# Performance work log

Hardware: AMD Instinct MI355X
Metric: run time of the kernel (lower is better)

## Reference

```python
import jax, jax.numpy as jnp
import numpy as np

B, T, C = 4, 2048, 1024
H, D = 16, 64  # num_heads, head_dim
P = 64         # prefix length


def setup_inputs() -> dict:
    key = jax.random.key(0)
    ks = jax.random.split(key, 12)
    s = 1.0 / np.sqrt(C)
    return {
        "x": jax.random.normal(ks[0], (B, T, C), dtype=jnp.float32),
        "attn_mask": jax.random.randint(ks[1], (B, 1, 1, T), 0, 2, dtype=jnp.int32),
        "prefix_k": jax.random.normal(ks[2], (B, H, P, D), dtype=jnp.float32),
        "prefix_v": jax.random.normal(ks[3], (B, H, P, D), dtype=jnp.float32),
        "Wq": jax.random.normal(ks[4], (C, C), dtype=jnp.float32) * s,
        "bq": jnp.zeros((C,), dtype=jnp.float32),
        "Wk": jax.random.normal(ks[5], (C, C), dtype=jnp.float32) * s,
        "bk": jnp.zeros((C,), dtype=jnp.float32),
        "Wv": jax.random.normal(ks[6], (C, C), dtype=jnp.float32) * s,
        "bv": jnp.zeros((C,), dtype=jnp.float32),
        "Wo": jax.random.normal(ks[7], (C, C), dtype=jnp.float32) * s,
        "bo": jnp.zeros((C,), dtype=jnp.float32),
    }


def _heads(y):
    # [B,T,C] -> [B,H,T,D]
    return y.reshape(B, T, H, D).transpose(0, 2, 1, 3)


def reference(x, attn_mask, prefix_k, prefix_v, Wq, bq, Wk, bk, Wv, bv, Wo, bo):
    q = _heads(x @ Wq.T + bq)
    k = _heads(x @ Wk.T + bk)
    v = _heads(x @ Wv.T + bv)
    # concat prefix K/V along key dim -> [B,H,P+T,D]
    k = jnp.concatenate([prefix_k, k], axis=2)
    v = jnp.concatenate([prefix_v, v], axis=2)
    # prefix positions are always visible
    prefix_mask = jnp.ones((B, 1, 1, P), dtype=attn_mask.dtype)
    mask = jnp.concatenate([prefix_mask, attn_mask], axis=-1)  # [B,1,1,P+T]
    scores = jnp.einsum('bhtd,bhsd->bhts', q, k) / jnp.sqrt(jnp.asarray(D, x.dtype))
    scores = jnp.where(mask == 0, -jnp.inf, scores)
    w = jax.nn.softmax(scores, axis=-1)
    o = jnp.einsum('bhts,bhsd->bhtd', w, v)
    o = o.transpose(0, 2, 1, 3).reshape(B, T, C)
    return o @ Wo.T + bo
```

## Files before the change

kernel.cpp:

```cpp
#include <hip/hip_runtime.h>
#include <hip/hip_bf16.h>

typedef __bf16 bf16;
typedef __attribute__((ext_vector_type(8))) __bf16 bf16x8;
typedef __attribute__((ext_vector_type(4))) __bf16 bf16x4;
typedef __attribute__((ext_vector_type(4))) float f32x4;
typedef __attribute__((ext_vector_type(16))) float f32x16;

#define MFMA16(a, b, c) __builtin_amdgcn_mfma_f32_16x16x32_bf16(a, b, c, 0, 0, 0)
#define MFMA32(a, b, c) __builtin_amdgcn_mfma_f32_32x32x16_bf16(a, b, c, 0, 0, 0)

__device__ __forceinline__ void gl_lds16(const void* g, void* l) {
    __builtin_amdgcn_global_load_lds(
        (const __attribute__((address_space(1))) void*)g,
        (__attribute__((address_space(3))) void*)l, 16, 0, 0);
}

#define QSCALE 0.18033688011f
#define LOGBIAS 24.0f

__global__ __launch_bounds__(256) void prep(
    const float* __restrict__ x, const float* __restrict__ Wq,
    const float* __restrict__ Wk, const float* __restrict__ Wv,
    const float* __restrict__ Wo, const float* __restrict__ pk,
    const float* __restrict__ pv, const int* __restrict__ mask,
    bf16* __restrict__ xb, bf16* __restrict__ wb,
    bf16* __restrict__ k_ws, bf16* __restrict__ vt_ws,
    int* __restrict__ ridx, int* __restrict__ nkv)
{
    const int blk = blockIdx.x, tid = threadIdx.x;
    if (blk < 4) {
        const int b = blk, lane = tid & 63, wv = tid >> 6;
        const int* mb = mask + b * 2048;
        int loc[8], s = 0;
#pragma unroll
        for (int e = 0; e < 8; ++e) { loc[e] = (mb[tid * 8 + e] != 0); s += loc[e]; }
        int inc = s;
#pragma unroll
        for (int off = 1; off < 64; off <<= 1) {
            int t = __shfl_up(inc, off);
            if (lane >= off) inc += t;
        }
        __shared__ int wt[4];
        if (lane == 63) wt[wv] = inc;
        __syncthreads();
        int wo = 0;
        for (int w = 0; w < wv; ++w) wo += wt[w];
        int excl = wo + inc - s;
#pragma unroll
        for (int e = 0; e < 8; ++e) {
            if (loc[e]) ridx[b * 2048 + excl] = tid * 8 + e;
            excl += loc[e];
        }
        if (tid == 255) nkv[b] = 64 + wo + inc;
    } else if (blk < 260) {
        int i = (blk - 4) * 256 + tid;
        {
            int base = i * 4;
            int bh = base >> 12, rem = base & 4095;
            float4 a = *(const float4*)&pk[base];
            bf16x4 ab;
            ab[0] = (bf16)a.x; ab[1] = (bf16)a.y; ab[2] = (bf16)a.z; ab[3] = (bf16)a.w;
            *(bf16x4*)&k_ws[(size_t)bh * (2112 * 64) + rem] = ab;
        }
        {
            int bh = i >> 10, r = i & 1023;
            int d = r >> 4, sq = (r & 15) * 4;
            bf16x4 vb;
#pragma unroll
            for (int e = 0; e < 4; ++e)
                vb[e] = (bf16)pv[(size_t)bh * 4096 + (sq + e) * 64 + d];
            *(bf16x4*)&vt_ws[((size_t)bh * 64 + d) * 2112 + sq] = vb;
        }
    } else {
        int i4 = (blk - 260) * 256 + tid;
        const float* src; bf16* dst; int off;
        if (i4 < 2097152) { src = x; dst = xb; off = i4; }
        else {
            int j = i4 - 2097152;
            int sel = j >> 18;
            off = j & 262143;
            src = (sel == 0) ? Wq : (sel == 1) ? Wk : (sel == 2) ? Wv : Wo;
            dst = wb + (size_t)sel * 1048576;
        }
        float4 a = *(const float4*)&src[(size_t)off * 4];
        bf16x4 o;
        o[0] = (bf16)a.x; o[1] = (bf16)a.y; o[2] = (bf16)a.z; o[3] = (bf16)a.w;
        *(bf16x4*)&dst[(size_t)off * 4] = o;
    }
}

__global__ __launch_bounds__(256) void proj_q_gemm(
    const bf16* __restrict__ X, const bf16* __restrict__ W,
    const float* __restrict__ bias, bf16* __restrict__ q_ws)
{
    __shared__ bf16 As[128 * 32];
    __shared__ bf16 Bs[128 * 32];
    const int m0 = blockIdx.x * 128, n0 = blockIdx.y * 128;
    const int tid = threadIdx.x, lane = tid & 63, wave = tid >> 6;
    const int ln = lane & 15, quad = lane >> 4;
    const int wr = (wave >> 1) * 64, wc = (wave & 1) * 64;
    const int srow = wave * 32 + (lane >> 2);
    const int scol = (lane & 3) * 8;

    const f32x4 z4 = {0.f, 0.f, 0.f, 0.f};
    f32x4 acc[4][4];
#pragma unroll
    for (int i = 0; i < 4; ++i)
#pragma unroll
        for (int j = 0; j < 4; ++j) acc[i][j] = z4;

    for (int k0 = 0; k0 < 1024; k0 += 32) {
        __syncthreads();
        gl_lds16(&X[(size_t)(m0 + srow) * 1024 + k0 + scol],      &As[(wave * 32) * 32]);
        gl_lds16(&X[(size_t)(m0 + srow + 16) * 1024 + k0 + scol], &As[(wave * 32 + 16) * 32]);
        gl_lds16(&W[(size_t)(n0 + srow) * 1024 + k0 + scol],      &Bs[(wave * 32) * 32]);
        gl_lds16(&W[(size_t)(n0 + srow + 16) * 1024 + k0 + scol], &Bs[(wave * 32 + 16) * 32]);
        __syncthreads();
        bf16x8 af[4], bfr[4];
#pragma unroll
        for (int i = 0; i < 4; ++i) af[i]  = *(const bf16x8*)&As[(wr + i * 16 + ln) * 32 + quad * 8];
#pragma unroll
        for (int j = 0; j < 4; ++j) bfr[j] = *(const bf16x8*)&Bs[(wc + j * 16 + ln) * 32 + quad * 8];
#pragma unroll
        for (int i = 0; i < 4; ++i)
#pragma unroll
            for (int j = 0; j < 4; ++j)
                acc[i][j] = MFMA16(af[i], bfr[j], acc[i][j]);
    }

#pragma unroll
    for (int j = 0; j < 4; ++j) {
        const int n = n0 + wc + j * 16 + ln;
        const float bb = bias[n];
        const int h = n >> 6, d = n & 63;
#pragma unroll
        for (int i = 0; i < 4; ++i) {
            int m = m0 + wr + i * 16 + quad * 4;
            int b = m >> 11, t = m & 2047;
#pragma unroll
            for (int r = 0; r < 4; ++r)
                q_ws[((size_t)(b * 16 + h) * 2048 + t + r) * 64 + d] =
                    (bf16)((acc[i][j][r] + bb) * QSCALE);
        }
    }
}

__global__ __launch_bounds__(256) void proj_kv_gemm(
    const bf16* __restrict__ X, const bf16* __restrict__ Wb,
    const float* __restrict__ bk, const float* __restrict__ bv,
    const int* __restrict__ ridx, const int* __restrict__ nkv,
    bf16* __restrict__ k_ws, bf16* __restrict__ vt_ws)
{
    const int bsel = blockIdx.x >> 4, tile = blockIdx.x & 15;
    const int nvis = nkv[bsel] - 64;
    const int mbase = tile * 128;
    if (mbase >= nvis) return;

    __shared__ bf16 As[128 * 32];
    __shared__ bf16 Bs[128 * 32];
    const int mode = blockIdx.z;
    const bf16* __restrict__ W = Wb + (size_t)(1 + mode) * 1048576;
    const float* __restrict__ bias = mode ? bv : bk;
    const int n0 = blockIdx.y * 128;
    const int tid = threadIdx.x, lane = tid & 63, wave = tid >> 6;
    const int ln = lane & 15, quad = lane >> 4;
    const int wr = (wave >> 1) * 64, wc = (wave & 1) * 64;
    const int srow = wave * 32 + (lane >> 2);
    const int scol = (lane & 3) * 8;

    int g0 = mbase + srow,      g1 = g0 + 16;
    int c0 = (g0 < nvis) ? g0 : nvis - 1;
    int c1 = (g1 < nvis) ? g1 : nvis - 1;
    const bf16* Xr0 = X + (size_t)(bsel * 2048 + ridx[bsel * 2048 + c0]) * 1024 + scol;
    const bf16* Xr1 = X + (size_t)(bsel * 2048 + ridx[bsel * 2048 + c1]) * 1024 + scol;

    const f32x4 z4 = {0.f, 0.f, 0.f, 0.f};
    f32x4 acc[4][4];
#pragma unroll
    for (int i = 0; i < 4; ++i)
#pragma unroll
        for (int j = 0; j < 4; ++j) acc[i][j] = z4;

    for (int k0 = 0; k0 < 1024; k0 += 32) {
        __syncthreads();
        gl_lds16(Xr0 + k0, &As[(wave * 32) * 32]);
        gl_lds16(Xr1 + k0, &As[(wave * 32 + 16) * 32]);
        gl_lds16(&W[(size_t)(n0 + srow) * 1024 + k0 + scol],      &Bs[(wave * 32) * 32]);
        gl_lds16(&W[(size_t)(n0 + srow + 16) * 1024 + k0 + scol], &Bs[(wave * 32 + 16) * 32]);
        __syncthreads();
        bf16x8 af[4], bfr[4];
#pragma unroll
        for (int i = 0; i < 4; ++i) af[i]  = *(const bf16x8*)&As[(wr + i * 16 + ln) * 32 + quad * 8];
#pragma unroll
        for (int j = 0; j < 4; ++j) bfr[j] = *(const bf16x8*)&Bs[(wc + j * 16 + ln) * 32 + quad * 8];
#pragma unroll
        for (int i = 0; i < 4; ++i)
#pragma unroll
            for (int j = 0; j < 4; ++j)
                acc[i][j] = MFMA16(af[i], bfr[j], acc[i][j]);
    }

#pragma unroll
    for (int j = 0; j < 4; ++j) {
        const int n = n0 + wc + j * 16 + ln;
        const float bb = bias[n];
        const int h = n >> 6, d = n & 63;
        const size_t bh64 = (size_t)(bsel * 16 + h);
#pragma unroll
        for (int i = 0; i < 4; ++i) {
            int ml = mbase + wr + i * 16 + quad * 4;
            if (mode == 0) {
#pragma unroll
                for (int r = 0; r < 4; ++r)
                    if (ml + r < nvis)
                        k_ws[(bh64 * 2112 + 64 + ml + r) * 64 + d] =
                            (bf16)(acc[i][j][r] + bb);
            } else {
                if (ml + 3 < nvis) {
                    bf16x4 pb;
#pragma unroll
                    for (int r = 0; r < 4; ++r) pb[r] = (bf16)(acc[i][j][r] + bb);
                    *(bf16x4*)&vt_ws[(bh64 * 64 + d) * 2112 + 64 + ml] = pb;
                } else {
#pragma unroll
                    for (int r = 0; r < 4; ++r)
                        if (ml + r < nvis)
                            vt_ws[(bh64 * 64 + d) * 2112 + 64 + ml + r] =
                                (bf16)(acc[i][j][r] + bb);
                }
            }
        }
    }
}

__global__ __launch_bounds__(256) void attn_kernel(
    const bf16* __restrict__ Q, const bf16* __restrict__ K,
    const bf16* __restrict__ VT, const int* __restrict__ nk,
    bf16* __restrict__ O)
{
    __shared__ bf16 Ks[64 * 72];
    __shared__ bf16 Vt[64 * 72];
    __shared__ bf16 Ps[4][32 * 72];
    const int tid = threadIdx.x, wave = tid >> 6, lane = tid & 63;
    const int ln = lane & 31, hh = lane >> 5;
    const int bh = blockIdx.y, b = bh >> 4, head = bh & 15;
    const bf16* __restrict__ Kb  = K  + (size_t)bh * (2112 * 64);
    const bf16* __restrict__ Vtb = VT + (size_t)bh * (64 * 2112);
    const int qg = blockIdx.x * 128 + wave * 32 + ln;
    const int nkeys = nk[b];
    const int send = ((nkeys + 63) >> 6) << 6;

    bf16x8 qf[4];
#pragma unroll
    for (int kt = 0; kt < 4; ++kt)
        qf[kt] = *(const bf16x8*)&Q[((size_t)bh * 2048 + qg) * 64 + kt * 16 + hh * 8];

    float l_r = 0.f;
    f32x16 acc[2];
#pragma unroll
    for (int r = 0; r < 16; ++r) { acc[0][r] = 0.f; acc[1][r] = 0.f; }

    const int ks_s = tid >> 3, ks_c = (tid & 7) * 8;
    const int vd = tid >> 3,  vs = (tid & 7) * 8;

    bf16x8 kr0, kr1, vr0, vr1;
    kr0 = *(const bf16x8*)&Kb[(size_t)ks_s * 64 + ks_c];
    kr1 = *(const bf16x8*)&Kb[(size_t)(ks_s + 32) * 64 + ks_c];
    vr0 = *(const bf16x8*)&Vtb[(size_t)vd * 2112 + vs];
    vr1 = *(const bf16x8*)&Vtb[(size_t)(vd + 32) * 2112 + vs];

    for (int s0 = 0; s0 < send; s0 += 64) {
        __syncthreads();
        *(bf16x8*)&Ks[ks_s * 72 + ks_c]        = kr0;
        *(bf16x8*)&Ks[(ks_s + 32) * 72 + ks_c] = kr1;
        *(bf16x8*)&Vt[vd * 72 + vs]            = vr0;
        *(bf16x8*)&Vt[(vd + 32) * 72 + vs]     = vr1;
        __syncthreads();

        if (s0 + 64 < send) {
            const int sn = s0 + 64;
            kr0 = *(const bf16x8*)&Kb[(size_t)(sn + ks_s) * 64 + ks_c];
            kr1 = *(const bf16x8*)&Kb[(size_t)(sn + ks_s + 32) * 64 + ks_c];
            vr0 = *(const bf16x8*)&Vtb[(size_t)vd * 2112 + sn + vs];
            vr1 = *(const bf16x8*)&Vtb[(size_t)(vd + 32) * 2112 + sn + vs];
        }

        f32x16 sc[2];
#pragma unroll
        for (int ts = 0; ts < 2; ++ts) {
            f32x16 s16;
#pragma unroll
            for (int r = 0; r < 16; ++r) s16[r] = 0.f;
#pragma unroll
            for (int kt = 0; kt < 4; ++kt) {
                bf16x8 kf = *(const bf16x8*)&Ks[(ts * 32 + ln) * 72 + kt * 16 + hh * 8];
                s16 = MFMA32(kf, qf[kt], s16);
            }
            sc[ts] = s16;
        }

        float rs = 0.f;
        if (s0 + 64 <= nkeys) {
#pragma unroll
            for (int ts = 0; ts < 2; ++ts)
#pragma unroll
                for (int rg = 0; rg < 4; ++rg) {
                    bf16x4 pb;
#pragma unroll
                    for (int i = 0; i < 4; ++i) {
                        float p = __builtin_amdgcn_exp2f(sc[ts][rg * 4 + i] - LOGBIAS);
                        rs += p;
                        pb[i] = (bf16)p;
                    }
                    *(bf16x4*)&Ps[wave][ln * 72 + ts * 32 + rg * 8 + hh * 4] = pb;
                }
        } else {
#pragma unroll
            for (int ts = 0; ts < 2; ++ts)
#pragma unroll
                for (int rg = 0; rg < 4; ++rg) {
                    bf16x4 pb;
#pragma unroll
                    for (int i = 0; i < 4; ++i) {
                        int key = s0 + ts * 32 + rg * 8 + hh * 4 + i;
                        float add = (key < nkeys) ? -LOGBIAS : -1e30f;
                        float p = __builtin_amdgcn_exp2f(sc[ts][rg * 4 + i] + add);
                        rs += p;
                        pb[i] = (bf16)p;
                    }
                    *(bf16x4*)&Ps[wave][ln * 72 + ts * 32 + rg * 8 + hh * 4] = pb;
                }
        }
        l_r += rs;

        __builtin_amdgcn_s_waitcnt(0xC07F);

        bf16x8 pf[4];
#pragma unroll
        for (int ss = 0; ss < 4; ++ss)
            pf[ss] = *(const bf16x8*)&Ps[wave][ln * 72 + ss * 16 + hh * 8];
#pragma unroll
        for (int ss = 0; ss < 4; ++ss) {
            bf16x8 v0 = *(const bf16x8*)&Vt[ln * 72 + ss * 16 + hh * 8];
            acc[0] = MFMA32(v0, pf[ss], acc[0]);
            bf16x8 v1 = *(const bf16x8*)&Vt[(32 + ln) * 72 + ss * 16 + hh * 8];
            acc[1] = MFMA32(v1, pf[ss], acc[1]);
        }
    }

    l_r += __shfl_xor(l_r, 32);
    float inv = 1.0f / l_r;
#pragma unroll
    for (int td = 0; td < 2; ++td)
#pragma unroll
        for (int rg = 0; rg < 4; ++rg) {
            bf16x4 ob;
#pragma unroll
            for (int i = 0; i < 4; ++i) ob[i] = (bf16)(acc[td][rg * 4 + i] * inv);
            *(bf16x4*)&Ps[wave][ln * 72 + td * 32 + rg * 8 + hh * 4] = ob;
        }
    __builtin_amdgcn_s_waitcnt(0xC07F);
    const int orow = lane >> 3, oc = (lane & 7) * 8;
#pragma unroll
    for (int pass = 0; pass < 4; ++pass) {
        int ml = pass * 8 + orow;
        bf16x8 ov = *(const bf16x8*)&Ps[wave][ml * 72 + oc];
        int qrow = blockIdx.x * 128 + wave * 32 + ml;
        *(bf16x8*)&O[((size_t)b * 2048 + qrow) * 1024 + head * 64 + oc] = ov;
    }
}

__global__ __launch_bounds__(256) void out_proj_gemm(
    const bf16* __restrict__ A, const bf16* __restrict__ W,
    const float* __restrict__ bias, float* __restrict__ out)
{
    __shared__ bf16 As[128 * 32];
    __shared__ bf16 Bs[128 * 32];
    const int m0 = blockIdx.x * 128, n0 = blockIdx.y * 128;
    const int tid = threadIdx.x, lane = tid & 63, wave = tid >> 6;
    const int ln = lane & 15, quad = lane >> 4;
    const int wr = (wave >> 1) * 64, wc = (wave & 1) * 64;
    const int srow = wave * 32 + (lane >> 2);
    const int scol = (lane & 3) * 8;

    const f32x4 z4 = {0.f, 0.f, 0.f, 0.f};
    f32x4 acc[4][4];
#pragma unroll
    for (int i = 0; i < 4; ++i)
#pragma unroll
        for (int j = 0; j < 4; ++j) acc[i][j] = z4;

    for (int k0 = 0; k0 < 1024; k0 += 32) {
        __syncthreads();
        gl_lds16(&A[(size_t)(m0 + srow) * 1024 + k0 + scol],      &As[(wave * 32) * 32]);
        gl_lds16(&A[(size_t)(m0 + srow + 16) * 1024 + k0 + scol], &As[(wave * 32 + 16) * 32]);
        gl_lds16(&W[(size_t)(n0 + srow) * 1024 + k0 + scol],      &Bs[(wave * 32) * 32]);
        gl_lds16(&W[(size_t)(n0 + srow + 16) * 1024 + k0 + scol], &Bs[(wave * 32 + 16) * 32]);
        __syncthreads();
        bf16x8 af[4], bfr[4];
#pragma unroll
        for (int i = 0; i < 4; ++i) af[i]  = *(const bf16x8*)&As[(wr + i * 16 + ln) * 32 + quad * 8];
#pragma unroll
        for (int j = 0; j < 4; ++j) bfr[j] = *(const bf16x8*)&Bs[(wc + j * 16 + ln) * 32 + quad * 8];
#pragma unroll
        for (int i = 0; i < 4; ++i)
#pragma unroll
            for (int j = 0; j < 4; ++j)
                acc[i][j] = MFMA16(af[i], bfr[j], acc[i][j]);
    }

#pragma unroll
    for (int j = 0; j < 4; ++j) {
        const int n = n0 + wc + j * 16 + ln;
        const float bb = bias[n];
#pragma unroll
        for (int i = 0; i < 4; ++i) {
#pragma unroll
            for (int r = 0; r < 4; ++r) {
                int m = m0 + wr + i * 16 + quad * 4 + r;
                out[(size_t)m * 1024 + n] = acc[i][j][r] + bb;
            }
        }
    }
}

extern "C" void kernel_launch(void* const* d_in, const int* in_sizes, int n_in,
                              void* d_out, int out_size, void* d_ws, size_t ws_size,
                              hipStream_t stream)
{
    const float* x    = (const float*)d_in[0];
    const int*   mask = (const int*)d_in[1];
    const float* pk   = (const float*)d_in[2];
    const float* pv   = (const float*)d_in[3];
    const float* Wq   = (const float*)d_in[4];
    const float* bq   = (const float*)d_in[5];
    const float* Wk   = (const float*)d_in[6];
    const float* bk   = (const float*)d_in[7];
    const float* Wv   = (const float*)d_in[8];
    const float* bv   = (const float*)d_in[9];
    const float* Wo   = (const float*)d_in[10];
    const float* bo   = (const float*)d_in[11];
    float* out = (float*)d_out;

    bf16* xb    = (bf16*)d_ws;
    bf16* wb    = xb + (size_t)8388608;
    bf16* q_ws  = wb + (size_t)4194304;
    bf16* k_ws  = q_ws + (size_t)8388608;
    bf16* vt_ws = k_ws + (size_t)8650752;
    int*  ridx  = (int*)(vt_ws + (size_t)8650752);
    int*  nkv   = ridx + 4 * 2048;
    bf16* a_ws  = xb;

    prep<<<dim3(12548), 256, 0, stream>>>(x, Wq, Wk, Wv, Wo, pk, pv, mask,
                                          xb, wb, k_ws, vt_ws, ridx, nkv);
    proj_q_gemm<<<dim3(64, 8), 256, 0, stream>>>(xb, wb, bq, q_ws);
    proj_kv_gemm<<<dim3(64, 8, 2), 256, 0, stream>>>(xb, wb, bk, bv, ridx, nkv,
                                                     k_ws, vt_ws);
    attn_kernel<<<dim3(16, 64), 256, 0, stream>>>(q_ws, k_ws, vt_ws, nkv, a_ws);
    out_proj_gemm<<<dim3(64, 8), 256, 0, stream>>>(a_ws, wb + (size_t)3 * 1048576,
                                                   bo, out);
}
```

Measured before the change: 275.3 us.

## Merge Q/K/V projection launches and keep P in registers for PV MFMA

The separate Q and K/V projection GEMM launches are fused into one flat-grid kernel that picks its role from the block index. This removes a launch and lets Q tiles overlap with the compacted K/V tiles. In the attention kernel, the V tile is written to LDS in a permuted column order so the softmax probabilities can feed the PV MFMA straight from registers. That drops the per-wave P LDS buffer, its store/load round trip and a waitcnt. The smaller LDS footprint may raise occupancy, but the permuted V store and the extra end-of-loop barrier add some cost.

```diff
diff --git a/kernel.cpp b/kernel.cpp
--- a/kernel.cpp
+++ b/kernel.cpp
@@ -90,90 +90,52 @@
     }
 }
 
-__global__ __launch_bounds__(256) void proj_q_gemm(
-    const bf16* __restrict__ X, const bf16* __restrict__ W,
-    const float* __restrict__ bias, bf16* __restrict__ q_ws)
+__global__ __launch_bounds__(256) void proj_gemm(
+    const bf16* __restrict__ X, const bf16* __restrict__ Wb,
+    const float* __restrict__ bq, const float* __restrict__ bk,
+    const float* __restrict__ bv, const int* __restrict__ ridx,
+    const int* __restrict__ nkv,
+    bf16* __restrict__ q_ws, bf16* __restrict__ k_ws, bf16* __restrict__ vt_ws)
 {
+    const int bx = blockIdx.x;
+    int kind, m0 = 0, n0, bsel = 0, nvis = 0, mbase = 0;
+    const bf16* W;
+    const float* bias;
+    if (bx < 512) {
+        kind = 0; m0 = (bx >> 3) * 128; n0 = (bx & 7) * 128;
+        W = Wb; bias = bq;
+    } else {
+        int j = bx - 512;
+        kind = 1 + (j >> 9);
+        int r = j & 511;
+        bsel = r >> 7;
+        mbase = ((r & 127) >> 3) * 128;
+        n0 = (r & 7) * 128;
+        nvis = nkv[bsel] - 64;
+        if (mbase >= nvis) return;
+        W = Wb + (size_t)kind * 1048576;
+        bias = (kind == 1) ? bk : bv;
+    }
+
     __shared__ bf16 As[128 * 32];
     __shared__ bf16 Bs[128 * 32];
-    const int m0 = blockIdx.x * 128, n0 = blockIdx.y * 128;
     const int tid = threadIdx.x, lane = tid & 63, wave = tid >> 6;
     const int ln = lane & 15, quad = lane >> 4;
     const int wr = (wave >> 1) * 64, wc = (wave & 1) * 64;
     const int srow = wave * 32 + (lane >> 2);
     const int scol = (lane & 3) * 8;
 
-    const f32x4 z4 = {0.f, 0.f, 0.f, 0.f};
-    f32x4 acc[4][4];
-#pragma unroll
-    for (int i = 0; i < 4; ++i)
-#pragma unroll
-        for (int j = 0; j < 4; ++j) acc[i][j] = z4;
-
-    for (int k0 = 0; k0 < 1024; k0 += 32) {
-        __syncthreads();
-        gl_lds16(&X[(size_t)(m0 + srow) * 1024 + k0 + scol],      &As[(wave * 32) * 32]);
-        gl_lds16(&X[(size_t)(m0 + srow + 16) * 1024 + k0 + scol], &As[(wave * 32 + 16) * 32]);
-        gl_lds16(&W[(size_t)(n0 + srow) * 1024 + k0 + scol],      &Bs[(wave * 32) * 32]);
-        gl_lds16(&W[(size_t)(n0 + srow + 16) * 1024 + k0 + scol], &Bs[(wave * 32 + 16) * 32]);
-        __syncthreads();
-        bf16x8 af[4], bfr[4];
-#pragma unroll
-        for (int i = 0; i < 4; ++i) af[i]  = *(const bf16x8*)&As[(wr + i * 16 + ln) * 32 + quad * 8];
-#pragma unroll
-        for (int j = 0; j < 4; ++j) bfr[j] = *(const bf16x8*)&Bs[(wc + j * 16 + ln) * 32 + quad * 8];
-#pragma unroll
-        for (int i = 0; i < 4; ++i)
-#pragma unroll
-            for (int j = 0; j < 4; ++j)
-                acc[i][j] = MFMA16(af[i], bfr[j], acc[i][j]);
-    }
-
-#pragma unroll
-    for (int j = 0; j < 4; ++j) {
-        const int n = n0 + wc + j * 16 + ln;
-        const float bb = bias[n];
-        const int h = n >> 6, d = n & 63;
-#pragma unroll
-        for (int i = 0; i < 4; ++i) {
-            int m = m0 + wr + i * 16 + quad * 4;
-            int b = m >> 11, t = m & 2047;
-#pragma unroll
-            for (int r = 0; r < 4; ++r)
-                q_ws[((size_t)(b * 16 + h) * 2048 + t + r) * 64 + d] =
-                    (bf16)((acc[i][j][r] + bb) * QSCALE);
-        }
-    }
-}
-
-__global__ __launch_bounds__(256) void proj_kv_gemm(
-    const bf16* __restrict__ X, const bf16* __restrict__ Wb,
-    const float* __restrict__ bk, const float* __restrict__ bv,
-    const int* __restrict__ ridx, const int* __restrict__ nkv,
-    bf16* __restrict__ k_ws, bf16* __restrict__ vt_ws)
-{
-    const int bsel = blockIdx.x >> 4, tile = blockIdx.x & 15;
-    const int nvis = nkv[bsel] - 64;
-    const int mbase = tile * 128;
-    if (mbase >= nvis) return;
-
-    __shared__ bf16 As[128 * 32];
-    __shared__ bf16 Bs[128 * 32];
-    const int mode = blockIdx.z;
-    const bf16* __restrict__ W = Wb + (size_t)(1 + mode) * 1048576;
-    const float* __restrict__ bias = mode ? bv : bk;
-    const int n0 = blockIdx.y * 128;
-    const int tid = threadIdx.x, lane = tid & 63, wave = tid >> 6;
-    const int ln = lane & 15, quad = lane >> 4;
-    const int wr = (wave >> 1) * 64, wc = (wave & 1) * 64;
-    const int srow = wave * 32 + (lane >> 2);
-    const int scol = (lane & 3) * 8;
-
-    int g0 = mbase + srow,      g1 = g0 + 16;
-    int c0 = (g0 < nvis) ? g0 : nvis - 1;
-    int c1 = (g1 < nvis) ? g1 : nvis - 1;
-    const bf16* Xr0 = X + (size_t)(bsel * 2048 + ridx[bsel * 2048 + c0]) * 1024 + scol;
-    const bf16* Xr1 = X + (size_t)(bsel * 2048 + ridx[bsel * 2048 + c1]) * 1024 + scol;
+    const bf16 *Xr0, *Xr1;
+    if (kind == 0) {
+        Xr0 = X + (size_t)(m0 + srow) * 1024 + scol;
+        Xr1 = Xr0 + (size_t)16 * 1024;
+    } else {
+        int g0 = mbase + srow, g1 = g0 + 16;
+        int c0 = (g0 < nvis) ? g0 : nvis - 1;
+        int c1 = (g1 < nvis) ? g1 : nvis - 1;
+        Xr0 = X + (size_t)(bsel * 2048 + ridx[bsel * 2048 + c0]) * 1024 + scol;
+        Xr1 = X + (size_t)(bsel * 2048 + ridx[bsel * 2048 + c1]) * 1024 + scol;
+    }
 
     const f32x4 z4 = {0.f, 0.f, 0.f, 0.f};
     f32x4 acc[4][4];
@@ -201,33 +163,51 @@
                 acc[i][j] = MFMA16(af[i], bfr[j], acc[i][j]);
     }
 
-#pragma unroll
-    for (int j = 0; j < 4; ++j) {
-        const int n = n0 + wc + j * 16 + ln;
-        const float bb = bias[n];
-        const int h = n >> 6, d = n & 63;
-        const size_t bh64 = (size_t)(bsel * 16 + h);
-#pragma unroll
-        for (int i = 0; i < 4; ++i) {
-            int ml = mbase + wr + i * 16 + quad * 4;
-            if (mode == 0) {
+    if (kind == 0) {
+#pragma unroll
+        for (int j = 0; j < 4; ++j) {
+            const int n = n0 + wc + j * 16 + ln;
+            const float bb = bias[n];
+            const int h = n >> 6, d = n & 63;
+#pragma unroll
+            for (int i = 0; i < 4; ++i) {
+                int m = m0 + wr + i * 16 + quad * 4;
+                int b = m >> 11, t = m & 2047;
 #pragma unroll
                 for (int r = 0; r < 4; ++r)
-                    if (ml + r < nvis)
-                        k_ws[(bh64 * 2112 + 64 + ml + r) * 64 + d] =
-                            (bf16)(acc[i][j][r] + bb);
-            } else {
-                if (ml + 3 < nvis) {
-                    bf16x4 pb;
-#pragma unroll
-                    for (int r = 0; r < 4; ++r) pb[r] = (bf16)(acc[i][j][r] + bb);
-                    *(bf16x4*)&vt_ws[(bh64 * 64 + d) * 2112 + 64 + ml] = pb;
-                } else {
+                    q_ws[((size_t)(b * 16 + h) * 2048 + t + r) * 64 + d] =
+                        (bf16)((acc[i][j][r] + bb) * QSCALE);
+            }
+        }
+    } else {
+#pragma unroll
+        for (int j = 0; j < 4; ++j) {
+            const int n = n0 + wc + j * 16 + ln;
+            const float bb = bias[n];
+            const int h = n >> 6, d = n & 63;
+            const size_t bh64 = (size_t)(bsel * 16 + h);
+#pragma unroll
+            for (int i = 0; i < 4; ++i) {
+                int ml = mbase + wr + i * 16 + quad * 4;
+                if (kind == 1) {
 #pragma unroll
                     for (int r = 0; r < 4; ++r)
                         if (ml + r < nvis)
-                            vt_ws[(bh64 * 64 + d) * 2112 + 64 + ml + r] =
+                            k_ws[(bh64 * 2112 + 64 + ml + r) * 64 + d] =
                                 (bf16)(acc[i][j][r] + bb);
+                } else {
+                    if (ml + 3 < nvis) {
+                        bf16x4 pb;
+#pragma unroll
+                        for (int r = 0; r < 4; ++r) pb[r] = (bf16)(acc[i][j][r] + bb);
+                        *(bf16x4*)&vt_ws[(bh64 * 64 + d) * 2112 + 64 + ml] = pb;
+                    } else {
+#pragma unroll
+                        for (int r = 0; r < 4; ++r)
+                            if (ml + r < nvis)
+                                vt_ws[(bh64 * 64 + d) * 2112 + 64 + ml + r] =
+                                    (bf16)(acc[i][j][r] + bb);
+                    }
                 }
             }
         }
@@ -239,9 +219,9 @@
     const bf16* __restrict__ VT, const int* __restrict__ nk,
     bf16* __restrict__ O)
 {
-    __shared__ bf16 Ks[64 * 72];
-    __shared__ bf16 Vt[64 * 72];
-    __shared__ bf16 Ps[4][32 * 72];
+    __shared__ bf16 smem[128 * 72];
+    bf16* Ks = smem;
+    bf16* Vt = smem + 64 * 72;
     const int tid = threadIdx.x, wave = tid >> 6, lane = tid & 63;
     const int ln = lane & 31, hh = lane >> 5;
     const int bh = blockIdx.y, b = bh >> 4, head = bh & 15;
@@ -262,7 +242,8 @@
     for (int r = 0; r < 16; ++r) { acc[0][r] = 0.f; acc[1][r] = 0.f; }
 
     const int ks_s = tid >> 3, ks_c = (tid & 7) * 8;
-    const int vd = tid >> 3,  vs = (tid & 7) * 8;
+    const int vd = tid >> 3, v8 = tid & 7, vs = v8 * 8;
+    const int vcb = (v8 >> 1) * 16 + ((v8 & 1) ? 4 : 0);
 
     bf16x8 kr0, kr1, vr0, vr1;
     kr0 = *(const bf16x8*)&Kb[(size_t)ks_s * 64 + ks_c];
@@ -274,8 +255,17 @@
         __syncthreads();
         *(bf16x8*)&Ks[ks_s * 72 + ks_c]        = kr0;
         *(bf16x8*)&Ks[(ks_s + 32) * 72 + ks_c] = kr1;
-        *(bf16x8*)&Vt[vd * 72 + vs]            = vr0;
-        *(bf16x8*)&Vt[(vd + 32) * 72 + vs]     = vr1;
+        {
+            bf16x4 lo, hi;
+#pragma unroll
+            for (int e = 0; e < 4; ++e) { lo[e] = vr0[e]; hi[e] = vr0[4 + e]; }
+            *(bf16x4*)&Vt[vd * 72 + vcb]     = lo;
+            *(bf16x4*)&Vt[vd * 72 + vcb + 8] = hi;
+#pragma unroll
+            for (int e = 0; e < 4; ++e) { lo[e] = vr1[e]; hi[e] = vr1[4 + e]; }
+            *(bf16x4*)&Vt[(vd + 32) * 72 + vcb]     = lo;
+            *(bf16x4*)&Vt[(vd + 32) * 72 + vcb + 8] = hi;
+        }
         __syncthreads();
 
         if (s0 + 64 < send) {
@@ -301,56 +291,47 @@
         }
 
         float rs = 0.f;
+        bf16x8 pf[4];
         if (s0 + 64 <= nkeys) {
 #pragma unroll
             for (int ts = 0; ts < 2; ++ts)
 #pragma unroll
-                for (int rg = 0; rg < 4; ++rg) {
-                    bf16x4 pb;
+                for (int rg = 0; rg < 4; ++rg)
 #pragma unroll
                     for (int i = 0; i < 4; ++i) {
                         float p = __builtin_amdgcn_exp2f(sc[ts][rg * 4 + i] - LOGBIAS);
                         rs += p;
-                        pb[i] = (bf16)p;
+                        pf[ts * 2 + (rg >> 1)][(rg & 1) * 4 + i] = (bf16)p;
                     }
-                    *(bf16x4*)&Ps[wave][ln * 72 + ts * 32 + rg * 8 + hh * 4] = pb;
-                }
         } else {
 #pragma unroll
             for (int ts = 0; ts < 2; ++ts)
 #pragma unroll
-                for (int rg = 0; rg < 4; ++rg) {
-                    bf16x4 pb;
+                for (int rg = 0; rg < 4; ++rg)
 #pragma unroll
                     for (int i = 0; i < 4; ++i) {
                         int key = s0 + ts * 32 + rg * 8 + hh * 4 + i;
                         float add = (key < nkeys) ? -LOGBIAS : -1e30f;
                         float p = __builtin_amdgcn_exp2f(sc[ts][rg * 4 + i] + add);
                         rs += p;
-                        pb[i] = (bf16)p;
+                        pf[ts * 2 + (rg >> 1)][(rg & 1) * 4 + i] = (bf16)p;
                     }
-                    *(bf16x4*)&Ps[wave][ln * 72 + ts * 32 + rg * 8 + hh * 4] = pb;
-                }
         }
         l_r += rs;
 
-        __builtin_amdgcn_s_waitcnt(0xC07F);
-
-        bf16x8 pf[4];
-#pragma unroll
-        for (int ss = 0; ss < 4; ++ss)
-            pf[ss] = *(const bf16x8*)&Ps[wave][ln * 72 + ss * 16 + hh * 8];
-#pragma unroll
-        for (int ss = 0; ss < 4; ++ss) {
-            bf16x8 v0 = *(const bf16x8*)&Vt[ln * 72 + ss * 16 + hh * 8];
-            acc[0] = MFMA32(v0, pf[ss], acc[0]);
-            bf16x8 v1 = *(const bf16x8*)&Vt[(32 + ln) * 72 + ss * 16 + hh * 8];
-            acc[1] = MFMA32(v1, pf[ss], acc[1]);
-        }
-    }
-
+#pragma unroll
+        for (int st = 0; st < 4; ++st) {
+            bf16x8 a0 = *(const bf16x8*)&Vt[ln * 72 + st * 16 + hh * 8];
+            acc[0] = MFMA32(a0, pf[st], acc[0]);
+            bf16x8 a1 = *(const bf16x8*)&Vt[(32 + ln) * 72 + st * 16 + hh * 8];
+            acc[1] = MFMA32(a1, pf[st], acc[1]);
+        }
+    }
+
+    __syncthreads();
     l_r += __shfl_xor(l_r, 32);
     float inv = 1.0f / l_r;
+    bf16* scratch = smem + wave * (32 * 72);
 #pragma unroll
     for (int td = 0; td < 2; ++td)
 #pragma unroll
@@ -358,14 +339,14 @@
             bf16x4 ob;
 #pragma unroll
             for (int i = 0; i < 4; ++i) ob[i] = (bf16)(acc[td][rg * 4 + i] * inv);
-            *(bf16x4*)&Ps[wave][ln * 72 + td * 32 + rg * 8 + hh * 4] = ob;
+            *(bf16x4*)&scratch[ln * 72 + td * 32 + rg * 8 + hh * 4] = ob;
         }
     __builtin_amdgcn_s_waitcnt(0xC07F);
     const int orow = lane >> 3, oc = (lane & 7) * 8;
 #pragma unroll
     for (int pass = 0; pass < 4; ++pass) {
         int ml = pass * 8 + orow;
-        bf16x8 ov = *(const bf16x8*)&Ps[wave][ml * 72 + oc];
+        bf16x8 ov = *(const bf16x8*)&scratch[ml * 72 + oc];
         int qrow = blockIdx.x * 128 + wave * 32 + ml;
         *(bf16x8*)&O[((size_t)b * 2048 + qrow) * 1024 + head * 64 + oc] = ov;
     }
@@ -454,9 +435,8 @@
 
     prep<<<dim3(12548), 256, 0, stream>>>(x, Wq, Wk, Wv, Wo, pk, pv, mask,
                                           xb, wb, k_ws, vt_ws, ridx, nkv);
-    proj_q_gemm<<<dim3(64, 8), 256, 0, stream>>>(xb, wb, bq, q_ws);
-    proj_kv_gemm<<<dim3(64, 8, 2), 256, 0, stream>>>(xb, wb, bk, bv, ridx, nkv,
-                                                     k_ws, vt_ws);
+    proj_gemm<<<dim3(1536), 256, 0, stream>>>(xb, wb, bq, bk, bv, ridx, nkv,
+                                              q_ws, k_ws, vt_ws);
     attn_kernel<<<dim3(16, 64), 256, 0, stream>>>(q_ws, k_ws, vt_ws, nkv, a_ws);
     out_proj_gemm<<<dim3(64, 8), 256, 0, stream>>>(a_ws, wb + (size_t)3 * 1048576,
                                                    bo, out);
```

After: 256.5 us. 6.8% less time.
